# Optimization experiments

Hardware: AMD Instinct MI355X
Metric: run time of the kernel (lower is better)

Reference implementation:

```python
import jax, jax.numpy as jnp
import numpy as np

B, D, C = 8192, 256, 128
MARGIN = 0.5
REPULSION_WEIGHT = 1.0
ALPHA = 0.5
BETA = 0.5
EPS = 1e-6  # F.pairwise_distance default eps, added to the difference vector


def make_centers(num_classes=C, embedding_dim=D):
    # center[k] is +/-1 one-hot along axis (k % embedding_dim)
    idx = np.arange(num_classes)
    centers = np.zeros((num_classes, embedding_dim), dtype=np.float32)
    centers[idx, idx % embedding_dim] = np.where(idx % 2 == 0, 1.0, -1.0)
    return jnp.asarray(centers)


def setup_inputs() -> dict:
    key = jax.random.key(0)
    k1, k2, k3 = jax.random.split(key, 3)
    features = jax.random.normal(k1, (B, D), dtype=jnp.float32)
    classification = jax.random.normal(k2, (B, C), dtype=jnp.float32)
    labels = jax.random.randint(k3, (B,), 0, C, dtype=jnp.int32)
    return {"features": features, "classification": classification, "labels": labels}


def _sculpted_loss(embeddings, labels, centers):
    b = embeddings.shape[0]
    # attractive: MSE to per-sample class center, mean over all elements
    center_targets = centers[labels]  # [B, D]
    attractive = jnp.mean((embeddings - center_targets) ** 2)

    # repulsive: for pairs i<j with different labels,
    # relu(margin - ||e_i - e_j + eps||_2)^2, summed then / (B(B-1)/2).
    sq_norm = jnp.sum(embeddings ** 2, axis=1)          # [B]
    row_sum = jnp.sum(embeddings, axis=1)               # [B]
    gram = embeddings @ embeddings.T                    # [B, B]
    sq = (sq_norm[:, None] + sq_norm[None, :] - 2.0 * gram
          + 2.0 * EPS * (row_sum[:, None] - row_sum[None, :])
          + embeddings.shape[1] * (EPS * EPS))
    dist = jnp.sqrt(jnp.maximum(sq, 1e-12))             # [B, B]

    iu = jnp.triu(jnp.ones((b, b), dtype=bool), k=1)    # i < j
    diff_label = labels[:, None] != labels[None, :]
    mask = iu & diff_label
    hinge = jnp.maximum(MARGIN - dist, 0.0)
    repulsive = jnp.sum(jnp.where(mask, hinge * hinge, 0.0))
    repulsive = repulsive / (b * (b - 1) / 2.0)

    return attractive + REPULSION_WEIGHT * repulsive


def reference(features, classification, labels):
    centers = make_centers()
    # cross entropy (mean over batch)
    logp = jax.nn.log_softmax(classification, axis=-1)
    ce = -jnp.mean(jnp.take_along_axis(logp, labels[:, None].astype(jnp.int32), axis=1)[:, 0])
    contrastive = _sculpted_loss(features, labels, centers)
    return BETA * contrastive + ALPHA * ce
```

## Files before the change

kernel.cpp:

```cpp
#include <hip/hip_runtime.h>
#include <stdint.h>

#define B_N   8192
#define D_DIM 256
#define C_CLS 128
#define EPSV  1e-6f
#define DEPS  (256.0f * EPSV * EPSV)
#define NT    64
#define NTRI  (NT * (NT + 1) / 2)

typedef float f32x4 __attribute__((ext_vector_type(4)));

__device__ __forceinline__ unsigned f2fp8(float v) {
    unsigned u = __float_as_uint(v);
    unsigned s = (u >> 24) & 0x80;
    unsigned a = u & 0x7fffffff;
    if (a > 0x43E00000u) a = 0x43E00000u;
    a += 0x7FFFF + ((a >> 20) & 1);
    int e = (int)(a >> 23) - 120;
    if (e <= 0) return s;
    return s | ((unsigned)e << 3) | ((a >> 20) & 7);
}


__global__ __launch_bounds__(256) void k_prep(
        const float* __restrict__ feat, const float* __restrict__ cls,
        const int* __restrict__ labels, unsigned char* __restrict__ e8,
        float* __restrict__ aR, float* __restrict__ bC,
        float* __restrict__ attrP, float* __restrict__ ceP) {
    int t = threadIdx.x, lane = t & 63, w = t >> 6;
    int row = blockIdx.x * 4 + w;
    int lab = labels[row];

    const float4* src = (const float4*)(feat + (size_t)row * D_DIM);
    float4 f = src[lane];
    unsigned pk = f2fp8(f.x) | (f2fp8(f.y) << 8) | (f2fp8(f.z) << 16) | (f2fp8(f.w) << 24);
    unsigned pkw = __shfl(pk, lane ^ ((row & 15) << 2));
    ((unsigned*)(e8 + (size_t)row * D_DIM))[lane] = pkw;

    float sq = f.x*f.x + f.y*f.y + f.z*f.z + f.w*f.w;
    float sm = f.x + f.y + f.z + f.w;
    float arr[4] = {f.x, f.y, f.z, f.w};
    float pick = ((lab >> 2) == lane) ? arr[lab & 3] : 0.f;

    const float2* csrc = (const float2*)(cls + (size_t)row * C_CLS);
    float2 c2 = csrc[lane];
    float mx = fmaxf(c2.x, c2.y);
    #pragma unroll
    for (int off = 32; off; off >>= 1) mx = fmaxf(mx, __shfl_xor(mx, off));
    float es = expf(c2.x - mx) + expf(c2.y - mx);
    float cpick = ((lab >> 1) == lane) ? ((lab & 1) ? c2.y : c2.x) : 0.f;

    #pragma unroll
    for (int off = 32; off; off >>= 1) {
        sq    += __shfl_xor(sq, off);
        sm    += __shfl_xor(sm, off);
        pick  += __shfl_xor(pick, off);
        es    += __shfl_xor(es, off);
        cpick += __shfl_xor(cpick, off);
    }
    __shared__ float wsumA[4], wsumC[4];
    if (lane == 0) {
        aR[row] = sq + 2.f * EPSV * sm;
        bC[row] = sq - 2.f * EPSV * sm + DEPS;
        float s = (lab & 1) ? -1.f : 1.f;
        wsumA[w] = sq - 2.f * s * pick + 1.f;
        wsumC[w] = -(cpick - mx - logf(es));
    }
    __syncthreads();
    if (t == 0) {
        attrP[blockIdx.x] = wsumA[0] + wsumA[1] + wsumA[2] + wsumA[3];
        ceP[blockIdx.x]   = wsumC[0] + wsumC[1] + wsumC[2] + wsumC[3];
    }
}

__global__ __launch_bounds__(256, 2) void k_gram(
        const unsigned char* __restrict__ e8, const float* __restrict__ aR,
        const float* __restrict__ bC, const int* __restrict__ labels,
        float* __restrict__ repP) {
    __shared__ __align__(16) unsigned char As[128 * 256];
    __shared__ __align__(16) unsigned char Bs[128 * 256];
    __shared__ float aM[128], bN[128];
    __shared__ int   lM[128], lN[128];
    __shared__ float wred[4];

    int t = threadIdx.x, lane = t & 63, w = t >> 6;

    int bid = blockIdx.x, tm = 0;
    while (bid >= NT - tm) { bid -= NT - tm; tm++; }
    int tn = tm + bid;

    if (t < 128) {
        int i = tm * 128 + t;
        aM[t] = aR[i]; lM[t] = labels[i];
    } else {
        int j = tn * 128 + (t - 128);
        bN[t - 128] = bC[j]; lN[t - 128] = labels[j];
    }

    #pragma unroll
    for (int i = 0; i < 8; i++) {
        const unsigned char* ga = e8 + (size_t)(tm * 128 + i * 16) * D_DIM + (t & 15) * 16
                                  + ((t >> 4) & 15) * 256;
        const unsigned char* gb = e8 + (size_t)(tn * 128 + i * 16) * D_DIM + (t & 15) * 16
                                  + ((t >> 4) & 15) * 256;
        __builtin_amdgcn_global_load_lds((const __attribute__((address_space(1))) void*)ga,
            (__attribute__((address_space(3))) void*)(As + i * 4096 + w * 1024), 16, 0, 0);
        __builtin_amdgcn_global_load_lds((const __attribute__((address_space(1))) void*)gb,
            (__attribute__((address_space(3))) void*)(Bs + i * 4096 + w * 1024), 16, 0, 0);
    }
    __syncthreads();

    f32x4 acc[4][4] = {};
    int wr = w >> 1, wc = w & 1;
    int quad = lane >> 4, l15 = lane & 15;
    int m0 = wr * 64, n0 = wc * 64;
    int half = (quad & 1) * 8, upair = quad >> 1;

    #pragma unroll
    for (int s = 0; s < 8; s++) {
        int ul = s * 2 + upair;
        long long av[4], bv[4];
        #pragma unroll
        for (int mi = 0; mi < 4; mi++) {
            int m = m0 + mi * 16 + l15;
            av[mi] = *(const long long*)(As + m * 256 + ((ul ^ l15) * 16) + half);
        }
        #pragma unroll
        for (int ni = 0; ni < 4; ni++) {
            int n = n0 + ni * 16 + l15;
            bv[ni] = *(const long long*)(Bs + n * 256 + ((ul ^ l15) * 16) + half);
        }
        #pragma unroll
        for (int mi = 0; mi < 4; mi++)
            #pragma unroll
            for (int ni = 0; ni < 4; ni++)
                acc[mi][ni] = __builtin_amdgcn_mfma_f32_16x16x32_fp8_fp8(av[mi], bv[ni], acc[mi][ni], 0, 0, 0);
    }

    float am[16], bn[4];
    #pragma unroll
    for (int ni = 0; ni < 4; ni++) bn[ni] = bN[wc * 64 + ni * 16 + l15];
    #pragma unroll
    for (int mi = 0; mi < 4; mi++)
        #pragma unroll
        for (int r = 0; r < 4; r++)
            am[mi * 4 + r] = aM[wr * 64 + mi * 16 + quad * 4 + r];

    float minv = 1e30f;
    #pragma unroll
    for (int mi = 0; mi < 4; mi++)
        #pragma unroll
        for (int ni = 0; ni < 4; ni++)
            #pragma unroll
            for (int r = 0; r < 4; r++)
                minv = fminf(minv, fmaf(-2.f, acc[mi][ni][r], am[mi * 4 + r] + bn[ni]));
    #pragma unroll
    for (int off = 32; off; off >>= 1) minv = fminf(minv, __shfl_xor(minv, off));

    float rep = 0.f;
    if (minv < 0.25f) {
        #pragma unroll
        for (int mi = 0; mi < 4; mi++) {
            #pragma unroll
            for (int ni = 0; ni < 4; ni++) {
                int n  = wc * 64 + ni * 16 + l15;
                int jg = tn * 128 + n;
                #pragma unroll
                for (int r = 0; r < 4; r++) {
                    int m  = wr * 64 + mi * 16 + quad * 4 + r;
                    int ig = tm * 128 + m;
                    float sq   = fmaf(-2.f, acc[mi][ni][r], am[mi * 4 + r] + bn[ni]);
                    float dist = sqrtf(fmaxf(sq, 1e-12f));
                    float h    = fmaxf(0.5f - dist, 0.f);
                    rep += (lM[m] != lN[n] && ig < jg) ? h * h : 0.f;
                }
            }
        }
        #pragma unroll
        for (int off = 32; off; off >>= 1) rep += __shfl_xor(rep, off);
    }
    if (lane == 0) wred[w] = rep;
    __syncthreads();
    if (t == 0) repP[blockIdx.x] = wred[0] + wred[1] + wred[2] + wred[3];
}

__global__ __launch_bounds__(256) void k_final(
        const float* __restrict__ P, float* __restrict__ out) {
    int t = threadIdx.x, lane = t & 63, w = t >> 6;
    float a = 0.f, c = 0.f, r = 0.f;
    for (int i = t; i < 2048; i += 256) { a += P[i]; c += P[2048 + i]; }
    for (int i = t; i < NTRI; i += 256) r += P[4096 + i];
    #pragma unroll
    for (int off = 32; off; off >>= 1) {
        a += __shfl_xor(a, off);
        c += __shfl_xor(c, off);
        r += __shfl_xor(r, off);
    }
    __shared__ float sa[4], sc[4], sr[4];
    if (lane == 0) { sa[w] = a; sc[w] = c; sr[w] = r; }
    __syncthreads();
    if (t == 0) {
        float attr = (sa[0] + sa[1] + sa[2] + sa[3]) / (float)((size_t)B_N * D_DIM);
        float ce   = (sc[0] + sc[1] + sc[2] + sc[3]) / (float)B_N;
        float rep  = (sr[0] + sr[1] + sr[2] + sr[3]) / ((float)B_N * (float)(B_N - 1) * 0.5f);
        out[0] = 0.5f * (attr + rep) + 0.5f * ce;
    }
}

extern "C" void kernel_launch(void* const* d_in, const int* in_sizes, int n_in,
                              void* d_out, int out_size, void* d_ws, size_t ws_size,
                              hipStream_t stream) {
    const float* feat   = (const float*)d_in[0];
    const float* cls    = (const float*)d_in[1];
    const int*   labels = (const int*)d_in[2];
    float* out = (float*)d_out;

    float*          P    = (float*)d_ws;
    unsigned char*  e8   = (unsigned char*)d_ws + 32768;
    float*          aR   = (float*)((char*)d_ws + 32768 + (size_t)B_N * D_DIM);
    float*          bC   = aR + B_N;
    float*          attrP = P;
    float*          ceP   = P + 2048;
    float*          repP  = P + 4096;

    k_prep <<<2048, 256, 0, stream>>>(feat, cls, labels, e8, aR, bC, attrP, ceP);
    k_gram <<<NTRI, 256, 0, stream>>>(e8, aR, bC, labels, repP);
    k_final<<<1, 256, 0, stream>>>(P, out);
}
```

Before: 98.86 us.

## Split gram K-loop into two LDS stages to halve shared memory and raise occupancy

The gram kernel now stages the FP8 operand tiles in two K-halves of 128 bytes per row instead of loading the full 256-byte rows at once. This halves LDS use and raises the launch bound from 2 to 4 blocks per CU, so more blocks can hide load latency. The prep kernel's swizzle changes to an XOR on bits 2-4 keyed by row&7, matching the new 128-byte row layout. It adds an extra barrier pair per K-half, and the load and compute phases are still serialized within a block.

```diff
diff --git a/kernel.cpp b/kernel.cpp
--- a/kernel.cpp
+++ b/kernel.cpp
@@ -35,8 +35,11 @@
     const float4* src = (const float4*)(feat + (size_t)row * D_DIM);
     float4 f = src[lane];
     unsigned pk = f2fp8(f.x) | (f2fp8(f.y) << 8) | (f2fp8(f.z) << 16) | (f2fp8(f.w) << 24);
-    unsigned pkw = __shfl(pk, lane ^ ((row & 15) << 2));
-    ((unsigned*)(e8 + (size_t)row * D_DIM))[lane] = pkw;
+    {
+        int s = (lane & 0x23) | (((((lane >> 2) & 7) ^ (row & 7))) << 2);
+        unsigned pkw = __shfl(pk, s);
+        ((unsigned*)(e8 + (size_t)row * D_DIM))[lane] = pkw;
+    }
 
     float sq = f.x*f.x + f.y*f.y + f.z*f.z + f.w*f.w;
     float sm = f.x + f.y + f.z + f.w;
@@ -74,12 +77,12 @@
     }
 }
 
-__global__ __launch_bounds__(256, 2) void k_gram(
+__global__ __launch_bounds__(256, 4) void k_gram(
         const unsigned char* __restrict__ e8, const float* __restrict__ aR,
         const float* __restrict__ bC, const int* __restrict__ labels,
         float* __restrict__ repP) {
-    __shared__ __align__(16) unsigned char As[128 * 256];
-    __shared__ __align__(16) unsigned char Bs[128 * 256];
+    __shared__ __align__(16) unsigned char As[128 * 128];
+    __shared__ __align__(16) unsigned char Bs[128 * 128];
     __shared__ float aM[128], bN[128];
     __shared__ int   lM[128], lN[128];
     __shared__ float wred[4];
@@ -98,44 +101,49 @@
         bN[t - 128] = bC[j]; lN[t - 128] = labels[j];
     }
 
-    #pragma unroll
-    for (int i = 0; i < 8; i++) {
-        const unsigned char* ga = e8 + (size_t)(tm * 128 + i * 16) * D_DIM + (t & 15) * 16
-                                  + ((t >> 4) & 15) * 256;
-        const unsigned char* gb = e8 + (size_t)(tn * 128 + i * 16) * D_DIM + (t & 15) * 16
-                                  + ((t >> 4) & 15) * 256;
-        __builtin_amdgcn_global_load_lds((const __attribute__((address_space(1))) void*)ga,
-            (__attribute__((address_space(3))) void*)(As + i * 4096 + w * 1024), 16, 0, 0);
-        __builtin_amdgcn_global_load_lds((const __attribute__((address_space(1))) void*)gb,
-            (__attribute__((address_space(3))) void*)(Bs + i * 4096 + w * 1024), 16, 0, 0);
-    }
-    __syncthreads();
+    int quad = lane >> 4, l15 = lane & 15;
+    int wr = w >> 1, wc = w & 1;
+    int m0 = wr * 64, n0 = wc * 64;
+    int upair = quad >> 1, h8 = (quad & 1) * 8;
+    int srow8 = t >> 3, scol = (t & 7) * 16;
 
     f32x4 acc[4][4] = {};
-    int wr = w >> 1, wc = w & 1;
-    int quad = lane >> 4, l15 = lane & 15;
-    int m0 = wr * 64, n0 = wc * 64;
-    int half = (quad & 1) * 8, upair = quad >> 1;
-
-    #pragma unroll
-    for (int s = 0; s < 8; s++) {
-        int ul = s * 2 + upair;
-        long long av[4], bv[4];
-        #pragma unroll
-        for (int mi = 0; mi < 4; mi++) {
-            int m = m0 + mi * 16 + l15;
-            av[mi] = *(const long long*)(As + m * 256 + ((ul ^ l15) * 16) + half);
+    #pragma unroll
+    for (int k0 = 0; k0 < 2; k0++) {
+        #pragma unroll
+        for (int i = 0; i < 4; i++) {
+            const unsigned char* ga = e8 + (size_t)(tm * 128 + i * 32 + srow8) * D_DIM
+                                      + k0 * 128 + scol;
+            const unsigned char* gb = e8 + (size_t)(tn * 128 + i * 32 + srow8) * D_DIM
+                                      + k0 * 128 + scol;
+            __builtin_amdgcn_global_load_lds((const __attribute__((address_space(1))) void*)ga,
+                (__attribute__((address_space(3))) void*)(As + i * 4096 + w * 1024), 16, 0, 0);
+            __builtin_amdgcn_global_load_lds((const __attribute__((address_space(1))) void*)gb,
+                (__attribute__((address_space(3))) void*)(Bs + i * 4096 + w * 1024), 16, 0, 0);
         }
-        #pragma unroll
-        for (int ni = 0; ni < 4; ni++) {
-            int n = n0 + ni * 16 + l15;
-            bv[ni] = *(const long long*)(Bs + n * 256 + ((ul ^ l15) * 16) + half);
+        __syncthreads();
+
+        #pragma unroll
+        for (int c = 0; c < 4; c++) {
+            int g0 = c * 2 + upair;
+            long long av[4], bv[4];
+            #pragma unroll
+            for (int mi = 0; mi < 4; mi++) {
+                int r = m0 + mi * 16 + l15;
+                av[mi] = *(const long long*)(As + r * 128 + ((g0 ^ (r & 7)) * 16) + h8);
+            }
+            #pragma unroll
+            for (int ni = 0; ni < 4; ni++) {
+                int r = n0 + ni * 16 + l15;
+                bv[ni] = *(const long long*)(Bs + r * 128 + ((g0 ^ (r & 7)) * 16) + h8);
+            }
+            #pragma unroll
+            for (int mi = 0; mi < 4; mi++)
+                #pragma unroll
+                for (int ni = 0; ni < 4; ni++)
+                    acc[mi][ni] = __builtin_amdgcn_mfma_f32_16x16x32_fp8_fp8(av[mi], bv[ni], acc[mi][ni], 0, 0, 0);
         }
-        #pragma unroll
-        for (int mi = 0; mi < 4; mi++)
-            #pragma unroll
-            for (int ni = 0; ni < 4; ni++)
-                acc[mi][ni] = __builtin_amdgcn_mfma_f32_16x16x32_fp8_fp8(av[mi], bv[ni], acc[mi][ni], 0, 0, 0);
+        __syncthreads();
     }
 
     float am[16], bn[4];
@@ -217,14 +225,11 @@
     float* out = (float*)d_out;
 
     float*          P    = (float*)d_ws;
-    unsigned char*  e8   = (unsigned char*)d_ws + 32768;
-    float*          aR   = (float*)((char*)d_ws + 32768 + (size_t)B_N * D_DIM);
+    unsigned char*  e8   = (unsigned char*)d_ws + 65536;
+    float*          aR   = (float*)((char*)d_ws + 65536 + (size_t)B_N * D_DIM);
     float*          bC   = aR + B_N;
-    float*          attrP = P;
-    float*          ceP   = P + 2048;
-    float*          repP  = P + 4096;
-
-    k_prep <<<2048, 256, 0, stream>>>(feat, cls, labels, e8, aR, bC, attrP, ceP);
-    k_gram <<<NTRI, 256, 0, stream>>>(e8, aR, bC, labels, repP);
+
+    k_prep <<<2048, 256, 0, stream>>>(feat, cls, labels, e8, aR, bC, P, P + 2048);
+    k_gram <<<NTRI, 256, 0, stream>>>(e8, aR, bC, labels, P + 4096);
     k_final<<<1, 256, 0, stream>>>(P, out);
 }
```

Measured after the change: 92.43 us, median of 2. 6.5% less time.
